# Performance work log

Measured on AMD Instinct MI355X. Metric: run time of the kernel, lower is better.

## Reference

```python
import jax, jax.numpy as jnp
import numpy as np

# footprints from the module: RB = 8-neighbor ring (center excluded), G = 4-neighbor cross
RB_OFFSETS = [(-1, -1), (-1, 0), (-1, 1), (0, -1), (0, 1), (1, -1), (1, 0), (1, 1)]
G_OFFSETS = [(-1, 0), (0, -1), (0, 1), (1, 0)]
N_ITER = 3


def _footprint_median(x, offsets):
    """scipy.ndimage.median_filter with a boolean footprint.
    scipy uses rank = n//2 of the sorted footprint values (no averaging for even n)
    and 'reflect' boundary mode (== numpy 'symmetric' padding).
    x: [B, H, W]
    """
    B, H, W = x.shape
    xp = jnp.pad(x, ((0, 0), (1, 1), (1, 1)), mode='symmetric')
    vals = jnp.stack([xp[:, 1 + dy:1 + dy + H, 1 + dx:1 + dx + W]
                      for dy, dx in offsets], axis=0)  # [n, B, H, W]
    n = len(offsets)
    return jnp.sort(vals, axis=0)[n // 2]


def _conv3(x, k):
    """3x3 conv with symmetric padding. x: [B,H,W], k: [3,3] -> [B,H,W]."""
    xp = jnp.pad(x, ((0, 0), (1, 1), (1, 1)), mode='symmetric')[:, None]  # [B,1,H+2,W+2]
    kern = k[None, None].astype(x.dtype)  # [1,1,3,3]
    out = jax.lax.conv_general_dilated(xp, kern, (1, 1), 'VALID')
    return out[:, 0]


def _demosaick(x):
    """Naive bilinear demosaick of a GRBG Bayer mosaic. x: [B,H,W] -> [B,3,H,W]."""
    B, H, W = x.shape
    yy, xx = jnp.meshgrid(jnp.arange(H), jnp.arange(W), indexing='ij')
    r_mask = ((yy % 2 == 0) & (xx % 2 == 1)).astype(x.dtype)
    b_mask = ((yy % 2 == 1) & (xx % 2 == 0)).astype(x.dtype)
    g_mask = 1.0 - r_mask - b_mask
    KG = jnp.array([[0., 1., 0.], [1., 4., 1.], [0., 1., 0.]]) / 4.0
    KRB = jnp.array([[1., 2., 1.], [2., 4., 2.], [1., 2., 1.]]) / 4.0
    R = _conv3(x * r_mask, KRB)
    G = _conv3(x * g_mask, KG)
    Bc = _conv3(x * b_mask, KRB)
    return jnp.stack([R, G, Bc], axis=1)


def reference(image):
    # image: [B, 1, H, W] Bayer mosaic
    d = _demosaick(image[:, 0])  # [B, 3, H, W]
    R, G, B = d[:, 0], d[:, 1], d[:, 2]
    for _ in range(N_ITER):
        # medians are non-differentiable in the original (numpy roundtrip)
        R = jax.lax.stop_gradient(_footprint_median(R - G, RB_OFFSETS)) + G
        B = jax.lax.stop_gradient(_footprint_median(B - G, RB_OFFSETS)) + G
        G = 0.5 * (jax.lax.stop_gradient(_footprint_median(G - R, G_OFFSETS))
                   + jax.lax.stop_gradient(_footprint_median(G - B, G_OFFSETS))
                   + R + B)
    return jnp.stack([R, G, B], axis=1)


def setup_inputs() -> dict:
    key = jax.random.key(0)
    image = jax.random.uniform(key, (8, 1, 1024, 1024), dtype=jnp.float32)
    return {"image": image}
```

## Files before the change

### kernel.cpp

```cpp
#include <hip/hip_runtime.h>

#define HH 1024
#define WW 1024
#define NB 8
constexpr int PLANE = HH * WW;

#define S   48
#define RG  46
#define NTX 32

typedef _Float16 h2 __attribute__((ext_vector_type(2)));

__device__ __forceinline__ int clampi(int v, int lo, int hi) {
    return v < lo ? lo : (v > hi ? hi : v);
}

union U2H { unsigned u; h2 h; };
__device__ __forceinline__ h2 u2h(unsigned v) { U2H x; x.u = v; return x.h; }
__device__ __forceinline__ unsigned h2u(h2 h) { U2H x; x.h = h; return x.u; }
__device__ __forceinline__ unsigned packdiff(float a, float b) {
    h2 h; h.x = (_Float16)a; h.y = (_Float16)b; return h2u(h);
}

__device__ __forceinline__ void cswap2(h2& a, h2& b) {
    h2 lo = __builtin_elementwise_min(a, b);
    b = __builtin_elementwise_max(a, b);
    a = lo;
}

__device__ __forceinline__ h2 med8p(h2 v0, h2 v1, h2 v2, h2 v3,
                                    h2 v4, h2 v5, h2 v6, h2 v7) {
    cswap2(v0, v1); cswap2(v2, v3); cswap2(v4, v5); cswap2(v6, v7);
    cswap2(v0, v2); cswap2(v1, v3); cswap2(v4, v6); cswap2(v5, v7);
    cswap2(v1, v2); cswap2(v5, v6);
    h2 p2 = __builtin_elementwise_min(v2, v6), p3 = __builtin_elementwise_min(v3, v7);
    h2 p4 = __builtin_elementwise_max(v0, v4), p5 = __builtin_elementwise_max(v1, v5);
    return __builtin_elementwise_max(__builtin_elementwise_min(p3, p5),
                                     __builtin_elementwise_max(p2, p4));
}

__device__ __forceinline__ h2 med4p(h2 a, h2 b, h2 c, h2 d) {
    h2 ab_hi = __builtin_elementwise_max(a, b), ab_lo = __builtin_elementwise_min(a, b);
    h2 cd_hi = __builtin_elementwise_max(c, d), cd_lo = __builtin_elementwise_min(c, d);
    return __builtin_elementwise_max(__builtin_elementwise_min(ab_hi, cd_hi),
                                     __builtin_elementwise_max(ab_lo, cd_lo));
}

__device__ __forceinline__ void demo_acc(float v, int pyn, int pxn, int ady, int adx,
                                         float& accR, float& accG, float& accB) {
    bool isr = (pyn == 0) && (pxn == 1);
    bool isb = (pyn == 1) && (pxn == 0);
    float wrb = 0.25f * (float)((2 - ady) * (2 - adx));
    int man = ady + adx;
    float wg = (man == 0) ? 1.0f : ((man == 1) ? 0.25f : 0.0f);
    accR += isr ? wrb * v : 0.0f;
    accB += isb ? wrb * v : 0.0f;
    accG += (!isr && !isb) ? wg * v : 0.0f;
}

template <int CA>
__device__ __forceinline__ void load4u(const unsigned* row, int c0, unsigned w[4]) {
    if constexpr (CA == 0) {
        uint4 q = *reinterpret_cast<const uint4*>(row + c0);
        w[0] = q.x; w[1] = q.y; w[2] = q.z; w[3] = q.w;
    } else {
        uint2 a = *reinterpret_cast<const uint2*>(row + c0);
        uint2 b = *reinterpret_cast<const uint2*>(row + c0 + 2);
        w[0] = a.x; w[1] = a.y; w[2] = b.x; w[3] = b.y;
    }
}
template <int CA>
__device__ __forceinline__ void load6u(const unsigned* row, int c0, unsigned w[6]) {
    if constexpr (CA == 0) {
        uint4 q = *reinterpret_cast<const uint4*>(row + c0);
        w[0] = row[c0 - 1];
        w[1] = q.x; w[2] = q.y; w[3] = q.z; w[4] = q.w;
        w[5] = row[c0 + 4];
    } else {
        uint4 a = *reinterpret_cast<const uint4*>(row + c0 - 2);
        uint4 b = *reinterpret_cast<const uint4*>(row + c0 + 2);
        w[0] = a.y; w[1] = a.z; w[2] = a.w; w[3] = b.x; w[4] = b.y; w[5] = b.z;
    }
}
template <int CA>
__device__ __forceinline__ void load4f(const float* row, int c0, float w[4]) {
    if constexpr (CA == 0) {
        float4 q = *reinterpret_cast<const float4*>(row + c0);
        w[0] = q.x; w[1] = q.y; w[2] = q.z; w[3] = q.w;
    } else {
        float2 a = *reinterpret_cast<const float2*>(row + c0);
        float2 b = *reinterpret_cast<const float2*>(row + c0 + 2);
        w[0] = a.x; w[1] = a.y; w[2] = b.x; w[3] = b.y;
    }
}
template <int CA>
__device__ __forceinline__ void store4f(float* row, int c0, const float v[4]) {
    if constexpr (CA == 0) {
        *reinterpret_cast<float4*>(row + c0) = make_float4(v[0], v[1], v[2], v[3]);
    } else {
        *reinterpret_cast<float2*>(row + c0) = make_float2(v[0], v[1]);
        *reinterpret_cast<float2*>(row + c0 + 2) = make_float2(v[2], v[3]);
    }
}
template <int CA>
__device__ __forceinline__ void store4u(unsigned* row, int c0, const unsigned v[4]) {
    if constexpr (CA == 0) {
        *reinterpret_cast<uint4*>(row + c0) = make_uint4(v[0], v[1], v[2], v[3]);
    } else {
        *reinterpret_cast<uint2*>(row + c0) = make_uint2(v[0], v[1]);
        *reinterpret_cast<uint2*>(row + c0 + 2) = make_uint2(v[2], v[3]);
    }
}

template <int R0, int NRP, int C0, int NG, int SH>
__device__ __forceinline__ void p1_int(const unsigned* __restrict__ sdRB,
                                       unsigned* __restrict__ uRB, int tid) {
    if (tid < NRP * NG) {
        int rp = tid / NG, g = tid - rp * NG;
        int r0 = R0 + 2 * rp;
        int B = (C0 - 1 - SH) + 4 * g;
        unsigned w[4][6];
#pragma unroll
        for (int i = 0; i < 4; ++i) {
            const unsigned* row = &sdRB[(r0 - 1 + i) * S + B];
            uint4 q0 = *reinterpret_cast<const uint4*>(row);
            uint4 q1 = *reinterpret_cast<const uint4*>(row + 4);
            unsigned e[8] = {q0.x, q0.y, q0.z, q0.w, q1.x, q1.y, q1.z, q1.w};
#pragma unroll
            for (int j = 0; j < 6; ++j) w[i][j] = e[SH + j];
        }
        int c0 = C0 + 4 * g;
#pragma unroll
        for (int rr = 0; rr < 2; ++rr) {
#pragma unroll
            for (int i = 0; i < 4; ++i) {
                h2 m = med8p(u2h(w[rr][i]), u2h(w[rr][i + 1]), u2h(w[rr][i + 2]),
                             u2h(w[rr + 1][i]), u2h(w[rr + 1][i + 2]),
                             u2h(w[rr + 2][i]), u2h(w[rr + 2][i + 1]), u2h(w[rr + 2][i + 2]));
                uRB[(r0 + rr) * S + c0 + i] = h2u(-m);
            }
        }
    }
}

template <int R0, int NRP, int C0, int NG, int CA, bool FINAL>
__device__ __forceinline__ void p2_int(float* __restrict__ sG, unsigned* __restrict__ sdRB,
                                       const unsigned* __restrict__ uRB, int tid,
                                       int y0, int x0,
                                       float* __restrict__ oR, float* __restrict__ oG,
                                       float* __restrict__ oB) {
    if (tid < NRP * NG) {
        int rp = tid / NG, g = tid - rp * NG;
        int r0 = R0 + 2 * rp;
        int c0 = C0 + 4 * g;
        unsigned wm[4], wp[4], w0[6], w1[6];
        load4u<CA>(&uRB[(r0 - 1) * S], c0, wm);
        load6u<CA>(&uRB[(r0) * S], c0, w0);
        load6u<CA>(&uRB[(r0 + 1) * S], c0, w1);
        load4u<CA>(&uRB[(r0 + 2) * S], c0, wp);
        float g0[4], g1[4];
        load4f<CA>(&sG[r0 * S], c0, g0);
        load4f<CA>(&sG[(r0 + 1) * S], c0, g1);
        float Rv[2][4], Gv[2][4], Bv[2][4];
#pragma unroll
        for (int i = 0; i < 4; ++i) {
            {
                h2 m = med4p(u2h(wm[i]), u2h(w0[i]), u2h(w0[i + 2]), u2h(w1[i + 1]));
                h2 uc = u2h(w0[i + 1]);
                float Gc = g0[i];
                float Rn = Gc - (float)uc.x, Bn = Gc - (float)uc.y;
                float Gn = 0.5f * ((float)m.x + (float)m.y + Rn + Bn);
                Rv[0][i] = Rn; Gv[0][i] = Gn; Bv[0][i] = Bn;
            }
            {
                h2 m = med4p(u2h(w0[i + 1]), u2h(w1[i]), u2h(w1[i + 2]), u2h(wp[i]));
                h2 uc = u2h(w1[i + 1]);
                float Gc = g1[i];
                float Rn = Gc - (float)uc.x, Bn = Gc - (float)uc.y;
                float Gn = 0.5f * ((float)m.x + (float)m.y + Rn + Bn);
                Rv[1][i] = Rn; Gv[1][i] = Gn; Bv[1][i] = Bn;
            }
        }
        if constexpr (FINAL) {
#pragma unroll
            for (int rr = 0; rr < 2; ++rr) {
                size_t o = (size_t)(y0 + r0 + rr) * WW + (x0 + c0);
                *reinterpret_cast<float4*>(&oR[o]) = make_float4(Rv[rr][0], Rv[rr][1], Rv[rr][2], Rv[rr][3]);
                *reinterpret_cast<float4*>(&oG[o]) = make_float4(Gv[rr][0], Gv[rr][1], Gv[rr][2], Gv[rr][3]);
                *reinterpret_cast<float4*>(&oB[o]) = make_float4(Bv[rr][0], Bv[rr][1], Bv[rr][2], Bv[rr][3]);
            }
        } else {
#pragma unroll
            for (int rr = 0; rr < 2; ++rr) {
                unsigned pd[4];
#pragma unroll
                for (int i = 0; i < 4; ++i)
                    pd[i] = packdiff(Rv[rr][i] - Gv[rr][i], Bv[rr][i] - Gv[rr][i]);
                store4f<CA>(&sG[(r0 + rr) * S], c0, Gv[rr]);
                store4u<CA>(&sdRB[(r0 + rr) * S], c0, pd);
            }
        }
    }
}

__device__ void p1_b(const unsigned* sdRB, unsigned* uRB, int tid,
                     int y0, int x0, int rlo, int nr, int clo, int nc) {
    for (int t = tid; t < nr * nc; t += 256) {
        int r = rlo + t / nc, c = clo + t - (t / nc) * nc;
        int gy = clampi(y0 + r, 0, HH - 1), gx = clampi(x0 + c, 0, WW - 1);
        int rm = clampi(gy - 1, 0, HH - 1) - y0, rp = clampi(gy + 1, 0, HH - 1) - y0;
        int cm = clampi(gx - 1, 0, WW - 1) - x0, cp = clampi(gx + 1, 0, WW - 1) - x0;
        h2 m = med8p(u2h(sdRB[rm * S + cm]), u2h(sdRB[rm * S + c]), u2h(sdRB[rm * S + cp]),
                     u2h(sdRB[r * S + cm]), u2h(sdRB[r * S + cp]),
                     u2h(sdRB[rp * S + cm]), u2h(sdRB[rp * S + c]), u2h(sdRB[rp * S + cp]));
        uRB[r * S + c] = h2u(-m);
    }
}

__device__ void p2_b(float* sG, unsigned* sdRB, const unsigned* uRB, int tid,
                     int y0, int x0, int rlo, int nr, int clo, int nc, bool fin,
                     float* oR, float* oG, float* oB) {
    for (int t = tid; t < nr * nc; t += 256) {
        int r = rlo + t / nc, c = clo + t - (t / nc) * nc;
        int gy = clampi(y0 + r, 0, HH - 1), gx = clampi(x0 + c, 0, WW - 1);
        int rm = clampi(gy - 1, 0, HH - 1) - y0, rp = clampi(gy + 1, 0, HH - 1) - y0;
        int cm = clampi(gx - 1, 0, WW - 1) - x0, cp = clampi(gx + 1, 0, WW - 1) - x0;
        h2 m = med4p(u2h(uRB[rm * S + c]), u2h(uRB[r * S + cm]),
                     u2h(uRB[r * S + cp]), u2h(uRB[rp * S + c]));
        h2 uc = u2h(uRB[r * S + c]);
        float Gc = sG[r * S + c];
        float Rn = Gc - (float)uc.x, Bn = Gc - (float)uc.y;
        float Gn = 0.5f * ((float)m.x + (float)m.y + Rn + Bn);
        if (fin) {
            size_t o = (size_t)(y0 + r) * WW + (x0 + c);
            oR[o] = Rn; oG[o] = Gn; oB[o] = Bn;
        } else {
            sG[r * S + c] = Gn;
            sdRB[r * S + c] = packdiff(Rn - Gn, Bn - Gn);
        }
    }
}

__global__ __launch_bounds__(256, 4) void fused_kernel(const float* __restrict__ img,
                                                       float* __restrict__ dst) {
    __shared__ __align__(16) unsigned smem[3 * RG * S];
    float* sI = reinterpret_cast<float*>(smem);
    unsigned* uRB = smem;
    unsigned* sdRB = smem + RG * S;
    float* sG = reinterpret_cast<float*>(smem + 2 * RG * S);

    int bx = blockIdx.x, by = blockIdx.y, bb = blockIdx.z;
    int x0 = bx * 32 - 8, y0 = by * 32 - 7;
    const float* im = img + (size_t)bb * PLANE;
    float* oR = dst + (size_t)bb * 3 * PLANE;
    float* oG = oR + PLANE;
    float* oB = oR + 2 * PLANE;
    int tid = threadIdx.x;
    bool interior = (bx >= 1 && bx <= 30 && by >= 1 && by <= 30);

    if (interior) {
        for (int t = tid; t < RG * 12; t += 256) {
            int r = t / 12, k = t - (t / 12) * 12;
            *reinterpret_cast<float4*>(&sI[r * S + 4 * k]) =
                *reinterpret_cast<const float4*>(&im[(size_t)(y0 + r) * WW + x0 + 4 * k]);
        }
        __syncthreads();
        if (tid < 242) {
            int qi = tid / 11, g = tid - (tid / 11) * 11;
            int rA = 1 + 2 * qi;
            int B = 4 * g;
            float w[4][6];
#pragma unroll
            for (int i = 0; i < 4; ++i) {
                const float* row = &sI[(rA - 1 + i) * S + B];
                float4 a = *reinterpret_cast<const float4*>(row);
                float4 b = *reinterpret_cast<const float4*>(row + 4);
                w[i][0] = a.y; w[i][1] = a.z; w[i][2] = a.w;
                w[i][3] = b.x; w[i][4] = b.y; w[i][5] = b.z;
            }
#pragma unroll
            for (int q = 0; q < 2; ++q) {
                int jb = 1 + 2 * q;
                float g00 = w[1][jb];
                float r00 = 0.5f * (w[1][jb - 1] + w[1][jb + 1]);
                float b00 = 0.5f * (w[0][jb] + w[2][jb]);
                float r01 = w[1][jb + 1];
                float g01 = 0.25f * (w[0][jb + 1] + w[2][jb + 1] + w[1][jb] + w[1][jb + 2]);
                float b01 = 0.25f * (w[0][jb] + w[0][jb + 2] + w[2][jb] + w[2][jb + 2]);
                float b10 = w[2][jb];
                float g10 = 0.25f * (w[1][jb] + w[3][jb] + w[2][jb - 1] + w[2][jb + 1]);
                float r10 = 0.25f * (w[1][jb - 1] + w[1][jb + 1] + w[3][jb - 1] + w[3][jb + 1]);
                float g11 = w[2][jb + 1];
                float r11 = 0.5f * (w[1][jb + 1] + w[3][jb + 1]);
                float b11 = 0.5f * (w[2][jb] + w[2][jb + 2]);
                int a0 = rA * S + 2 + 4 * g + 2 * q;
                *reinterpret_cast<float2*>(&sG[a0]) = make_float2(g00, g01);
                *reinterpret_cast<float2*>(&sG[a0 + S]) = make_float2(g10, g11);
                *reinterpret_cast<uint2*>(&sdRB[a0]) =
                    make_uint2(packdiff(r00 - g00, b00 - g00), packdiff(r01 - g01, b01 - g01));
                *reinterpret_cast<uint2*>(&sdRB[a0 + S]) =
                    make_uint2(packdiff(r10 - g10, b10 - g10), packdiff(r11 - g11, b11 - g11));
            }
        }
        __syncthreads();
        p1_int<2, 21, 3, 11, 2>(sdRB, uRB, tid);
        __syncthreads();
        p2_int<3, 20, 4, 10, 0, false>(sG, sdRB, uRB, tid, y0, x0, oR, oG, oB);
        __syncthreads();
        p1_int<4, 19, 5, 10, 0>(sdRB, uRB, tid);
        __syncthreads();
        p2_int<5, 18, 6, 9, 2, false>(sG, sdRB, uRB, tid, y0, x0, oR, oG, oB);
        __syncthreads();
        p1_int<6, 17, 7, 9, 2>(sdRB, uRB, tid);
        __syncthreads();
        p2_int<7, 16, 8, 8, 0, true>(sG, sdRB, uRB, tid, y0, x0, oR, oG, oB);
    } else {
        for (int t = tid; t < RG * S; t += 256) {
            int r = t / S, c = t - (t / S) * S;
            int gy = clampi(y0 + r, 0, HH - 1), gx = clampi(x0 + c, 0, WW - 1);
            sI[r * S + c] = im[(size_t)gy * WW + gx];
        }
        __syncthreads();
        {
            for (int t = tid; t < 44 * 44; t += 256) {
                int r = 1 + t / 44, c = 2 + t - (t / 44) * 44;
                int gy = clampi(y0 + r, 0, HH - 1), gx = clampi(x0 + c, 0, WW - 1);
                float accR = 0.f, accG = 0.f, accB = 0.f;
#pragma unroll
                for (int dy = -1; dy <= 1; ++dy)
#pragma unroll
                    for (int dx = -1; dx <= 1; ++dx) {
                        int cy = clampi(gy + dy, 0, HH - 1);
                        int cx = clampi(gx + dx, 0, WW - 1);
                        float v = sI[(cy - y0) * S + (cx - x0)];
                        demo_acc(v, cy & 1, cx & 1, dy < 0 ? -dy : dy, dx < 0 ? -dx : dx,
                                 accR, accG, accB);
                    }
                sG[r * S + c] = accG;
                sdRB[r * S + c] = packdiff(accR - accG, accB - accG);
            }
        }
        __syncthreads();
        p1_b(sdRB, uRB, tid, y0, x0, 2, 42, 3, 42);
        __syncthreads();
        p2_b(sG, sdRB, uRB, tid, y0, x0, 3, 40, 4, 40, false, oR, oG, oB);
        __syncthreads();
        p1_b(sdRB, uRB, tid, y0, x0, 4, 38, 5, 38);
        __syncthreads();
        p2_b(sG, sdRB, uRB, tid, y0, x0, 5, 36, 6, 36, false, oR, oG, oB);
        __syncthreads();
        p1_b(sdRB, uRB, tid, y0, x0, 6, 34, 7, 34);
        __syncthreads();
        p2_b(sG, sdRB, uRB, tid, y0, x0, 7, 32, 8, 32, true, oR, oG, oB);
    }
}

extern "C" void kernel_launch(void* const* d_in, const int* in_sizes, int n_in,
                              void* d_out, int out_size, void* d_ws, size_t ws_size,
                              hipStream_t stream) {
    const float* img = (const float*)d_in[0];
    float* out = (float*)d_out;
    dim3 block(256);
    dim3 grid(NTX, NTX, NB);
    fused_kernel<<<grid, block, 0, stream>>>(img, out);
}
```

Baseline: 148.7 us.

## Store G plane in fp16 shared memory, widen row stride, vectorize median stores

The shared G buffer changes from fp32 to fp16, which cuts its LDS footprint and traffic. The row stride grows from 48 to 52, apparently to spread accesses across LDS banks. p1_int now covers aligned column groups and writes each group of four results with vector stores. Keeping G in fp16 across iterations adds rounding error to the final output, and the wider stride uses more shared memory per row.

```diff
diff --git a/kernel.cpp b/kernel.cpp
--- a/kernel.cpp
+++ b/kernel.cpp
@@ -5,7 +5,7 @@
 #define NB 8
 constexpr int PLANE = HH * WW;
 
-#define S   48
+#define S   52
 #define RG  46
 #define NTX 32
 
@@ -83,26 +83,6 @@
     }
 }
 template <int CA>
-__device__ __forceinline__ void load4f(const float* row, int c0, float w[4]) {
-    if constexpr (CA == 0) {
-        float4 q = *reinterpret_cast<const float4*>(row + c0);
-        w[0] = q.x; w[1] = q.y; w[2] = q.z; w[3] = q.w;
-    } else {
-        float2 a = *reinterpret_cast<const float2*>(row + c0);
-        float2 b = *reinterpret_cast<const float2*>(row + c0 + 2);
-        w[0] = a.x; w[1] = a.y; w[2] = b.x; w[3] = b.y;
-    }
-}
-template <int CA>
-__device__ __forceinline__ void store4f(float* row, int c0, const float v[4]) {
-    if constexpr (CA == 0) {
-        *reinterpret_cast<float4*>(row + c0) = make_float4(v[0], v[1], v[2], v[3]);
-    } else {
-        *reinterpret_cast<float2*>(row + c0) = make_float2(v[0], v[1]);
-        *reinterpret_cast<float2*>(row + c0 + 2) = make_float2(v[2], v[3]);
-    }
-}
-template <int CA>
 __device__ __forceinline__ void store4u(unsigned* row, int c0, const unsigned v[4]) {
     if constexpr (CA == 0) {
         *reinterpret_cast<uint4*>(row + c0) = make_uint4(v[0], v[1], v[2], v[3]);
@@ -111,40 +91,53 @@
         *reinterpret_cast<uint2*>(row + c0 + 2) = make_uint2(v[2], v[3]);
     }
 }
-
-template <int R0, int NRP, int C0, int NG, int SH>
+__device__ __forceinline__ void load4h(const _Float16* rowp, int c0, float g[4]) {
+    h2 a = *reinterpret_cast<const h2*>(rowp + c0);
+    h2 b = *reinterpret_cast<const h2*>(rowp + c0 + 2);
+    g[0] = (float)a.x; g[1] = (float)a.y; g[2] = (float)b.x; g[3] = (float)b.y;
+}
+__device__ __forceinline__ void store4h(_Float16* rowp, int c0, const float v[4]) {
+    h2 a; a.x = (_Float16)v[0]; a.y = (_Float16)v[1];
+    h2 b; b.x = (_Float16)v[2]; b.y = (_Float16)v[3];
+    *reinterpret_cast<h2*>(rowp + c0) = a;
+    *reinterpret_cast<h2*>(rowp + c0 + 2) = b;
+}
+
+template <int R0, int NRP, int C0, int NG>
 __device__ __forceinline__ void p1_int(const unsigned* __restrict__ sdRB,
                                        unsigned* __restrict__ uRB, int tid) {
+    static_assert((C0 & 3) == 2, "p1_int needs C0 % 4 == 2");
     if (tid < NRP * NG) {
         int rp = tid / NG, g = tid - rp * NG;
         int r0 = R0 + 2 * rp;
-        int B = (C0 - 1 - SH) + 4 * g;
+        int c0 = C0 + 4 * g;
+        int B = c0 - 2;
         unsigned w[4][6];
 #pragma unroll
         for (int i = 0; i < 4; ++i) {
             const unsigned* row = &sdRB[(r0 - 1 + i) * S + B];
             uint4 q0 = *reinterpret_cast<const uint4*>(row);
             uint4 q1 = *reinterpret_cast<const uint4*>(row + 4);
-            unsigned e[8] = {q0.x, q0.y, q0.z, q0.w, q1.x, q1.y, q1.z, q1.w};
-#pragma unroll
-            for (int j = 0; j < 6; ++j) w[i][j] = e[SH + j];
-        }
-        int c0 = C0 + 4 * g;
+            w[i][0] = q0.y; w[i][1] = q0.z; w[i][2] = q0.w;
+            w[i][3] = q1.x; w[i][4] = q1.y; w[i][5] = q1.z;
+        }
 #pragma unroll
         for (int rr = 0; rr < 2; ++rr) {
+            unsigned rv[4];
 #pragma unroll
             for (int i = 0; i < 4; ++i) {
                 h2 m = med8p(u2h(w[rr][i]), u2h(w[rr][i + 1]), u2h(w[rr][i + 2]),
                              u2h(w[rr + 1][i]), u2h(w[rr + 1][i + 2]),
                              u2h(w[rr + 2][i]), u2h(w[rr + 2][i + 1]), u2h(w[rr + 2][i + 2]));
-                uRB[(r0 + rr) * S + c0 + i] = h2u(-m);
-            }
+                rv[i] = h2u(-m);
+            }
+            store4u<2>(&uRB[(r0 + rr) * S], c0, rv);
         }
     }
 }
 
 template <int R0, int NRP, int C0, int NG, int CA, bool FINAL>
-__device__ __forceinline__ void p2_int(float* __restrict__ sG, unsigned* __restrict__ sdRB,
+__device__ __forceinline__ void p2_int(_Float16* __restrict__ sG, unsigned* __restrict__ sdRB,
                                        const unsigned* __restrict__ uRB, int tid,
                                        int y0, int x0,
                                        float* __restrict__ oR, float* __restrict__ oG,
@@ -159,8 +152,8 @@
         load6u<CA>(&uRB[(r0 + 1) * S], c0, w1);
         load4u<CA>(&uRB[(r0 + 2) * S], c0, wp);
         float g0[4], g1[4];
-        load4f<CA>(&sG[r0 * S], c0, g0);
-        load4f<CA>(&sG[(r0 + 1) * S], c0, g1);
+        load4h(&sG[r0 * S], c0, g0);
+        load4h(&sG[(r0 + 1) * S], c0, g1);
         float Rv[2][4], Gv[2][4], Bv[2][4];
 #pragma unroll
         for (int i = 0; i < 4; ++i) {
@@ -196,7 +189,7 @@
 #pragma unroll
                 for (int i = 0; i < 4; ++i)
                     pd[i] = packdiff(Rv[rr][i] - Gv[rr][i], Bv[rr][i] - Gv[rr][i]);
-                store4f<CA>(&sG[(r0 + rr) * S], c0, Gv[rr]);
+                store4h(&sG[(r0 + rr) * S], c0, Gv[rr]);
                 store4u<CA>(&sdRB[(r0 + rr) * S], c0, pd);
             }
         }
@@ -217,7 +210,7 @@
     }
 }
 
-__device__ void p2_b(float* sG, unsigned* sdRB, const unsigned* uRB, int tid,
+__device__ void p2_b(_Float16* sG, unsigned* sdRB, const unsigned* uRB, int tid,
                      int y0, int x0, int rlo, int nr, int clo, int nc, bool fin,
                      float* oR, float* oG, float* oB) {
     for (int t = tid; t < nr * nc; t += 256) {
@@ -228,14 +221,14 @@
         h2 m = med4p(u2h(uRB[rm * S + c]), u2h(uRB[r * S + cm]),
                      u2h(uRB[r * S + cp]), u2h(uRB[rp * S + c]));
         h2 uc = u2h(uRB[r * S + c]);
-        float Gc = sG[r * S + c];
+        float Gc = (float)sG[r * S + c];
         float Rn = Gc - (float)uc.x, Bn = Gc - (float)uc.y;
         float Gn = 0.5f * ((float)m.x + (float)m.y + Rn + Bn);
         if (fin) {
             size_t o = (size_t)(y0 + r) * WW + (x0 + c);
             oR[o] = Rn; oG[o] = Gn; oB[o] = Bn;
         } else {
-            sG[r * S + c] = Gn;
+            sG[r * S + c] = (_Float16)Gn;
             sdRB[r * S + c] = packdiff(Rn - Gn, Bn - Gn);
         }
     }
@@ -243,11 +236,11 @@
 
 __global__ __launch_bounds__(256, 4) void fused_kernel(const float* __restrict__ img,
                                                        float* __restrict__ dst) {
-    __shared__ __align__(16) unsigned smem[3 * RG * S];
-    float* sI = reinterpret_cast<float*>(smem);
+    __shared__ __align__(16) unsigned smem[3 * RG * S / 2 * 2 - RG * S / 2 + RG * S];
     unsigned* uRB = smem;
     unsigned* sdRB = smem + RG * S;
-    float* sG = reinterpret_cast<float*>(smem + 2 * RG * S);
+    _Float16* sG = reinterpret_cast<_Float16*>(smem + 2 * RG * S);
+    float* sI = reinterpret_cast<float*>(smem);
 
     int bx = blockIdx.x, by = blockIdx.y, bb = blockIdx.z;
     int x0 = bx * 32 - 8, y0 = by * 32 - 7;
@@ -294,8 +287,10 @@
                 float r11 = 0.5f * (w[1][jb + 1] + w[3][jb + 1]);
                 float b11 = 0.5f * (w[2][jb] + w[2][jb + 2]);
                 int a0 = rA * S + 2 + 4 * g + 2 * q;
-                *reinterpret_cast<float2*>(&sG[a0]) = make_float2(g00, g01);
-                *reinterpret_cast<float2*>(&sG[a0 + S]) = make_float2(g10, g11);
+                h2 gh0; gh0.x = (_Float16)g00; gh0.y = (_Float16)g01;
+                h2 gh1; gh1.x = (_Float16)g10; gh1.y = (_Float16)g11;
+                *reinterpret_cast<h2*>(&sG[a0]) = gh0;
+                *reinterpret_cast<h2*>(&sG[a0 + S]) = gh1;
                 *reinterpret_cast<uint2*>(&sdRB[a0]) =
                     make_uint2(packdiff(r00 - g00, b00 - g00), packdiff(r01 - g01, b01 - g01));
                 *reinterpret_cast<uint2*>(&sdRB[a0 + S]) =
@@ -303,15 +298,15 @@
             }
         }
         __syncthreads();
-        p1_int<2, 21, 3, 11, 2>(sdRB, uRB, tid);
+        p1_int<2, 21, 2, 11>(sdRB, uRB, tid);
         __syncthreads();
         p2_int<3, 20, 4, 10, 0, false>(sG, sdRB, uRB, tid, y0, x0, oR, oG, oB);
         __syncthreads();
-        p1_int<4, 19, 5, 10, 0>(sdRB, uRB, tid);
+        p1_int<4, 19, 2, 11>(sdRB, uRB, tid);
         __syncthreads();
         p2_int<5, 18, 6, 9, 2, false>(sG, sdRB, uRB, tid, y0, x0, oR, oG, oB);
         __syncthreads();
-        p1_int<6, 17, 7, 9, 2>(sdRB, uRB, tid);
+        p1_int<6, 17, 6, 9>(sdRB, uRB, tid);
         __syncthreads();
         p2_int<7, 16, 8, 8, 0, true>(sG, sdRB, uRB, tid, y0, x0, oR, oG, oB);
     } else {
@@ -336,7 +331,7 @@
                         demo_acc(v, cy & 1, cx & 1, dy < 0 ? -dy : dy, dx < 0 ? -dx : dx,
                                  accR, accG, accB);
                     }
-                sG[r * S + c] = accG;
+                sG[r * S + c] = (_Float16)accG;
                 sdRB[r * S + c] = packdiff(accR - accG, accB - accG);
             }
         }
```

After: 162.7 us. +9.4%, slower.
